# Kernel optimization log

Hardware: AMD Instinct MI355X
Metric: run time of the kernel (lower is better)

Reference implementation:

```python
import math
import jax, jax.numpy as jnp
import numpy as np


def fwht(x):
    """Vectorized batched fast Walsh-Hadamard transform, faithful to the
    torch cat/slice butterfly: x is [B, D], D a power of 2."""
    B, D = x.shape
    n_stages = int(math.log2(D))
    y = x[:, :, None]  # [B, D, 1]
    for _ in range(n_stages):
        even = y[:, 0::2]  # [B, D/2, k]
        odd = y[:, 1::2]
        # concat along last dim: (even+odd, even-odd) -> [B, D/2, 2k]
        y = jnp.concatenate([even + odd, even - odd], axis=2)
    # final shape [B, 1, D] -> squeeze
    return y[:, 0, :]


def setup_inputs() -> dict:
    key = jax.random.key(0)
    x = jax.random.normal(key, (16384, 4096), dtype=jnp.float32)
    return {"x": x}


def reference(x) -> jnp.ndarray:
    return fwht(x)
```

## Files before the change

### kernel.cpp

```cpp
#include <hip/hip_runtime.h>


typedef float f32x4 __attribute__((ext_vector_type(4)));

__device__ __forceinline__ void wht16(float v[16]) {
#pragma unroll
    for (int h = 1; h < 16; h <<= 1) {
#pragma unroll
        for (int i = 0; i < 16; i++) {
            if ((i & h) == 0) {
                float a = v[i];
                float b = v[i ^ h];
                v[i]     = a + b;
                v[i ^ h] = a - b;
            }
        }
    }
}

__global__ __launch_bounds__(256) void fwht4096_kernel(const float* __restrict__ in,
                                                       float* __restrict__ out) {
    __shared__ float lds[256 * 17];

    const int row = blockIdx.x;
    const int t   = threadIdx.x;

    float v[16];

    const f32x4* p4 = (const f32x4*)(in + (size_t)row * 4096 + t * 16);
#pragma unroll
    for (int q = 0; q < 4; q++) {
        f32x4 f = p4[q];
        v[4 * q + 0] = f.x;
        v[4 * q + 1] = f.y;
        v[4 * q + 2] = f.z;
        v[4 * q + 3] = f.w;
    }

    wht16(v);

#pragma unroll
    for (int r = 0; r < 16; r++) lds[t * 17 + r] = v[r];
    __syncthreads();

    const int u_hi = t >> 4;
    const int u_lo = t & 15;
#pragma unroll
    for (int k = 0; k < 16; k++) v[k] = lds[(u_hi * 16 + k) * 17 + u_lo];

    wht16(v);

#pragma unroll
    for (int k = 0; k < 16; k++) lds[(u_hi * 16 + k) * 17 + u_lo] = v[k];
    __syncthreads();

#pragma unroll
    for (int m = 0; m < 16; m++) v[m] = lds[(m * 16 + u_hi) * 17 + u_lo];

    wht16(v);

#pragma unroll
    for (int m = 0; m < 16; m++) lds[(m * 16 + u_hi) * 17 + u_lo] = v[m];
    __syncthreads();

#pragma unroll
    for (int r = 0; r < 16; r++) v[r] = lds[t * 17 + r];

    f32x4* op4 = (f32x4*)(out + (size_t)row * 4096 + t * 16);
#pragma unroll
    for (int q = 0; q < 4; q++) {
        f32x4 f = { v[4 * q + 0], v[4 * q + 1], v[4 * q + 2], v[4 * q + 3] };
        op4[q] = f;
    }
}

extern "C" void kernel_launch(void* const* d_in, const int* in_sizes, int n_in,
                              void* d_out, int out_size, void* d_ws, size_t ws_size,
                              hipStream_t stream) {
    const float* x = (const float*)d_in[0];
    float* out     = (float*)d_out;
    const int rows = in_sizes[0] / 4096;
    fwht4096_kernel<<<dim3(rows), dim3(256), 0, stream>>>(x, out);
}
```

Baseline: 111.8 us.

## Replace two LDS transposes with DPP/swizzle cross-lane butterflies and swizzled LDS layout

```diff
diff --git a/kernel.cpp b/kernel.cpp
--- a/kernel.cpp
+++ b/kernel.cpp
@@ -2,6 +2,9 @@
 
 
 typedef float f32x4 __attribute__((ext_vector_type(4)));
+
+#define DPP_XOR(x, ctrl) \
+    __int_as_float(__builtin_amdgcn_mov_dpp(__float_as_int(x), (ctrl), 0xF, 0xF, true))
 
 __device__ __forceinline__ void wht16(float v[16]) {
 #pragma unroll
@@ -9,8 +12,7 @@
 #pragma unroll
         for (int i = 0; i < 16; i++) {
             if ((i & h) == 0) {
-                float a = v[i];
-                float b = v[i ^ h];
+                float a = v[i], b = v[i ^ h];
                 v[i]     = a + b;
                 v[i ^ h] = a - b;
             }
@@ -20,10 +22,16 @@
 
 __global__ __launch_bounds__(256) void fwht4096_kernel(const float* __restrict__ in,
                                                        float* __restrict__ out) {
-    __shared__ float lds[256 * 17];
+    __shared__ float lds[4096];
 
     const int row = blockIdx.x;
     const int t   = threadIdx.x;
+    const int l01 = t & 3, l23 = (t >> 2) & 3, l45 = (t >> 4) & 3, w = t >> 6;
+
+    const float s1  = (t & 1)  ? -1.f : 1.f;
+    const float s2  = (t & 2)  ? -1.f : 1.f;
+    const float s16 = (t & 16) ? -1.f : 1.f;
+    const float s32 = (t & 32) ? -1.f : 1.f;
 
     float v[16];
 
@@ -31,47 +39,66 @@
 #pragma unroll
     for (int q = 0; q < 4; q++) {
         f32x4 f = p4[q];
-        v[4 * q + 0] = f.x;
-        v[4 * q + 1] = f.y;
-        v[4 * q + 2] = f.z;
-        v[4 * q + 3] = f.w;
+        v[4 * q + 0] = f.x; v[4 * q + 1] = f.y;
+        v[4 * q + 2] = f.z; v[4 * q + 3] = f.w;
     }
 
     wht16(v);
 
 #pragma unroll
-    for (int r = 0; r < 16; r++) lds[t * 17 + r] = v[r];
+    for (int r = 0; r < 16; r++) {
+        float p = DPP_XOR(v[r], 0xB1);
+        v[r] = fmaf(s1, v[r], p);
+    }
+#pragma unroll
+    for (int r = 0; r < 16; r++) {
+        float p = DPP_XOR(v[r], 0x4E);
+        v[r] = fmaf(s2, v[r], p);
+    }
+
+    {
+        const int xw = ((w & 3) << 3) ^ ((l45 & 3) << 2);
+        float* wrow  = &lds[(t ^ (xw >> 4)) * 16];
+        const int bx = (xw >> 2) & 3;
+#pragma unroll
+        for (int a = 0; a < 4; a++) {
+            f32x4 f = { v[4 * a + 0], v[4 * a + 1], v[4 * a + 2], v[4 * a + 3] };
+            *(f32x4*)&wrow[4 * (a ^ bx)] = f;
+        }
+    }
     __syncthreads();
 
-    const int u_hi = t >> 4;
-    const int u_lo = t & 15;
+    {
+        const int low = w * 16 + l23 * 4 + l01;
 #pragma unroll
-    for (int k = 0; k < 16; k++) v[k] = lds[(u_hi * 16 + k) * 17 + u_lo];
+        for (int g = 0; g < 4; g++) {
+            const int base = l45 * 1024 + ((low ^ (l45 << 3)) ^ (g << 2));
+#pragma unroll
+            for (int i = 0; i < 4; i++) {
+                const int r = 4 * g + i;
+                v[r] = lds[base + r * 64];
+            }
+        }
+    }
 
     wht16(v);
 
 #pragma unroll
-    for (int k = 0; k < 16; k++) lds[(u_hi * 16 + k) * 17 + u_lo] = v[k];
-    __syncthreads();
+    for (int r = 0; r < 16; r++) {
+        float p = __int_as_float(
+            __builtin_amdgcn_ds_swizzle(__float_as_int(v[r]), 0x401F));
+        v[r] = fmaf(s16, v[r], p);
+    }
 
 #pragma unroll
-    for (int m = 0; m < 16; m++) v[m] = lds[(m * 16 + u_hi) * 17 + u_lo];
+    for (int r = 0; r < 16; r++) {
+        float p = __shfl_xor(v[r], 32, 64);
+        v[r] = fmaf(s32, v[r], p);
+    }
 
-    wht16(v);
-
+    float* ob = out + (size_t)row * 4096 + l45 * 1024 + w * 16 + l23 * 4 + l01;
 #pragma unroll
-    for (int m = 0; m < 16; m++) lds[(m * 16 + u_hi) * 17 + u_lo] = v[m];
-    __syncthreads();
-
-#pragma unroll
-    for (int r = 0; r < 16; r++) v[r] = lds[t * 17 + r];
-
-    f32x4* op4 = (f32x4*)(out + (size_t)row * 4096 + t * 16);
-#pragma unroll
-    for (int q = 0; q < 4; q++) {
-        f32x4 f = { v[4 * q + 0], v[4 * q + 1], v[4 * q + 2], v[4 * q + 3] };
-        op4[q] = f;
-    }
+    for (int r = 0; r < 16; r++) ob[r * 64] = v[r];
 }
 
 extern "C" void kernel_launch(void* const* d_in, const int* in_sizes, int n_in,
```

Result: faster. 101.2 us (-9.4%).

## Process two rows per block and store final stage directly to global

Applied to the files above, without the earlier changes.

```diff
diff --git a/kernel.cpp b/kernel.cpp
--- a/kernel.cpp
+++ b/kernel.cpp
@@ -9,8 +9,7 @@
 #pragma unroll
         for (int i = 0; i < 16; i++) {
             if ((i & h) == 0) {
-                float a = v[i];
-                float b = v[i ^ h];
+                float a = v[i], b = v[i ^ h];
                 v[i]     = a + b;
                 v[i ^ h] = a - b;
             }
@@ -18,33 +17,16 @@
     }
 }
 
-__global__ __launch_bounds__(256) void fwht4096_kernel(const float* __restrict__ in,
-                                                       float* __restrict__ out) {
-    __shared__ float lds[256 * 17];
-
-    const int row = blockIdx.x;
-    const int t   = threadIdx.x;
-
-    float v[16];
-
-    const f32x4* p4 = (const f32x4*)(in + (size_t)row * 4096 + t * 16);
-#pragma unroll
-    for (int q = 0; q < 4; q++) {
-        f32x4 f = p4[q];
-        v[4 * q + 0] = f.x;
-        v[4 * q + 1] = f.y;
-        v[4 * q + 2] = f.z;
-        v[4 * q + 3] = f.w;
-    }
+__device__ __forceinline__ void process_row(float v[16], float* lds, int t,
+                                            float* __restrict__ outrow) {
+    const int u_hi = t >> 4;
+    const int u_lo = t & 15;
 
     wht16(v);
 
 #pragma unroll
     for (int r = 0; r < 16; r++) lds[t * 17 + r] = v[r];
     __syncthreads();
-
-    const int u_hi = t >> 4;
-    const int u_lo = t & 15;
 #pragma unroll
     for (int k = 0; k < 16; k++) v[k] = lds[(u_hi * 16 + k) * 17 + u_lo];
 
@@ -53,25 +35,48 @@
 #pragma unroll
     for (int k = 0; k < 16; k++) lds[(u_hi * 16 + k) * 17 + u_lo] = v[k];
     __syncthreads();
-
 #pragma unroll
     for (int m = 0; m < 16; m++) v[m] = lds[(m * 16 + u_hi) * 17 + u_lo];
 
     wht16(v);
 
 #pragma unroll
-    for (int m = 0; m < 16; m++) lds[(m * 16 + u_hi) * 17 + u_lo] = v[m];
+    for (int m = 0; m < 16; m++) outrow[m * 256 + t] = v[m];
+}
+
+__global__ __launch_bounds__(256) void fwht4096x2_kernel(const float* __restrict__ in,
+                                                         float* __restrict__ out) {
+    __shared__ float lds[256 * 17];
+
+    const int t = threadIdx.x;
+    const size_t base = (size_t)blockIdx.x * 2 * 4096;
+
+    const f32x4* pa = (const f32x4*)(in + base + t * 16);
+    const f32x4* pb = (const f32x4*)(in + base + 4096 + t * 16);
+
+    f32x4 fa[4], fb[4];
+#pragma unroll
+    for (int q = 0; q < 4; q++) fa[q] = pa[q];
+#pragma unroll
+    for (int q = 0; q < 4; q++) fb[q] = pb[q];
+
+    float v[16];
+
+#pragma unroll
+    for (int q = 0; q < 4; q++) {
+        v[4 * q + 0] = fa[q].x; v[4 * q + 1] = fa[q].y;
+        v[4 * q + 2] = fa[q].z; v[4 * q + 3] = fa[q].w;
+    }
+    process_row(v, lds, t, out + base);
+
     __syncthreads();
 
 #pragma unroll
-    for (int r = 0; r < 16; r++) v[r] = lds[t * 17 + r];
-
-    f32x4* op4 = (f32x4*)(out + (size_t)row * 4096 + t * 16);
-#pragma unroll
     for (int q = 0; q < 4; q++) {
-        f32x4 f = { v[4 * q + 0], v[4 * q + 1], v[4 * q + 2], v[4 * q + 3] };
-        op4[q] = f;
+        v[4 * q + 0] = fb[q].x; v[4 * q + 1] = fb[q].y;
+        v[4 * q + 2] = fb[q].z; v[4 * q + 3] = fb[q].w;
     }
+    process_row(v, lds, t, out + base + 4096);
 }
 
 extern "C" void kernel_launch(void* const* d_in, const int* in_sizes, int n_in,
@@ -80,5 +85,5 @@
     const float* x = (const float*)d_in[0];
     float* out     = (float*)d_out;
     const int rows = in_sizes[0] / 4096;
-    fwht4096_kernel<<<dim3(rows), dim3(256), 0, stream>>>(x, out);
+    fwht4096x2_kernel<<<dim3(rows / 2), dim3(256), 0, stream>>>(x, out);
 }
```

Measured after the change: 104.4 us. -6.6%, faster.
